# Kernel tuning notes

Hardware: AMD Instinct MI355X
Metric: run time of the kernel (lower is better)

## Reference

```python
import jax, jax.numpy as jnp
import numpy as np

DIM = 512
NUM_HEADS = 8
HEAD_DIM = DIM // NUM_HEADS
EPS = 1e-05
BETA_INIT, TEMP_INIT, SHARP_INIT = 1.0, 0.5, 4.0


def setup_inputs() -> dict:
    key = jax.random.key(0)
    ks = jax.random.split(key, 9)
    b, t = 2, 1024
    s = 1.0 / np.sqrt(DIM)
    inp = {
        "x": jax.random.normal(ks[0], (b, t, DIM), dtype=jnp.float32),
        "wq_k": jax.random.normal(ks[1], (DIM, DIM), dtype=jnp.float32) * s,
        "wq_b": jnp.zeros((DIM,), dtype=jnp.float32),
        "wk_k": jax.random.normal(ks[2], (DIM, DIM), dtype=jnp.float32) * s,
        "wk_b": jnp.zeros((DIM,), dtype=jnp.float32),
        "wv_k": jax.random.normal(ks[3], (DIM, DIM), dtype=jnp.float32) * s,
        "wv_b": jnp.zeros((DIM,), dtype=jnp.float32),
        "wo_k": jax.random.normal(ks[4], (DIM, DIM), dtype=jnp.float32) * s,
        "wo_b": jnp.zeros((DIM,), dtype=jnp.float32),
        "log_beta": jnp.full((NUM_HEADS,), np.log(BETA_INIT), dtype=jnp.float32),
        "log_temp": jnp.full((NUM_HEADS,), np.log(TEMP_INIT), dtype=jnp.float32),
        "log_sharp": jnp.full((NUM_HEADS,), np.log(SHARP_INIT), dtype=jnp.float32),
    }
    return inp


def _softplus(x, beta):
    return (1.0 / beta) * jnp.log(1.0 + jnp.exp(beta * x))


def _combine(a, b):
    # log-domain combine: elements m (b,h,t,n), log_N (b,h,t,p,n), log_D (b,h,t,n)
    m_x, ln_x, ld_x = a
    m_y, ln_y, ld_y = b
    m_new = jnp.maximum(m_x, m_y)
    dx = m_x - m_new
    dy = m_y - m_new
    # note: (..., None) broadcast onto (b,h,t,p,n) works because p == n == HEAD_DIM
    ln_new = jnp.logaddexp(ln_x + dx[..., None], ln_y + dy[..., None])
    ld_new = jnp.logaddexp(ld_x + dx, ld_y + dy)
    return (m_new, ln_new, ld_new)


def reference(x, wq_k, wq_b, wk_k, wk_b, wv_k, wv_b, wo_k, wo_b,
              log_beta, log_temp, log_sharp):
    b, t, _ = x.shape
    q = (x @ wq_k + wq_b).reshape(b, t, NUM_HEADS, HEAD_DIM).transpose(0, 2, 1, 3)
    k = (x @ wk_k + wk_b).reshape(b, t, NUM_HEADS, HEAD_DIM).transpose(0, 2, 1, 3)
    v = (x @ wv_k + wv_b).reshape(b, t, NUM_HEADS, HEAD_DIM).transpose(0, 2, 1, 3)

    beta = jnp.exp(log_beta)[:, None, None]   # (h,1,1)
    temp = jnp.exp(log_temp)[:, None, None]
    sharp = jnp.exp(log_sharp)[:, None, None]

    q = q / temp
    k = k / temp
    Qf = _softplus(q, beta)  # (b,h,t,n)
    Kf = _softplus(k, beta)

    m0 = jnp.log(Kf + EPS)                         # (b,h,t,n)
    N0 = jnp.einsum('bhtp,bhtn->bhtpn', v, Kf)     # (b,h,t,p,n)
    D0 = Kf                                        # (b,h,t,n)

    m_c, N_c, D_c = jax.lax.associative_scan(_combine, (m0, N0, D0), axis=2)

    Y_num = jnp.einsum('bhtp,bhtpq->bhtq', Qf, N_c)
    Y_den = jnp.einsum('bhtp,bhtp->bht', Qf, D_c)
    Y = Y_num / (Y_den[..., None] + EPS)           # (b,h,t,n)
    Y = jnp.sign(Y) * jnp.abs(Y) ** sharp

    pos = (jnp.arange(1, t + 1, dtype=Y.dtype) / t).reshape(1, 1, t, 1)
    Y = Y * pos

    Y = Y.transpose(0, 2, 1, 3).reshape(b, t, DIM)
    return Y @ wo_k + wo_b
```

## Files before the change

### kernel.cpp

```cpp
#include <hip/hip_runtime.h>
#include <hip/hip_bf16.h>
#include <math.h>

#define DIM 512
#define NH 8
#define HD 64
#define TT 1024
#define CH 64
#define CL 16
#define EPSF 1e-5f
#define LN2F 0.69314718056f
#define LOG2EF 1.44269504089f

typedef unsigned short ushort_t;
typedef __attribute__((ext_vector_type(8))) short bf16x8;
typedef __attribute__((ext_vector_type(4))) float f32x4;

__device__ __forceinline__ float fexp2(float x) { return __builtin_amdgcn_exp2f(x); }
__device__ __forceinline__ float flog2(float x) { return __builtin_amdgcn_logf(x); }

__device__ __forceinline__ ushort_t f2bf(float f) {
    union { float f; unsigned u; } v; v.f = f;
    unsigned r = v.u + 0x7FFFu + ((v.u >> 16) & 1u);
    return (ushort_t)(r >> 16);
}
__device__ __forceinline__ float bf2f(ushort_t h) {
    union { unsigned u; float f; } v; v.u = ((unsigned)h) << 16;
    return v.f;
}

#define NXB 1024
__launch_bounds__(256)
__global__ void k_cvt(const float* __restrict__ x, ushort_t* __restrict__ xh,
                      ushort_t* __restrict__ xl,
                      const float* __restrict__ wq, const float* __restrict__ wk,
                      const float* __restrict__ wv, const float* __restrict__ wo,
                      ushort_t* __restrict__ wTh, ushort_t* __restrict__ wTl,
                      ushort_t* __restrict__ wTo)
{
    if (blockIdx.x < NXB) {
        int i = (blockIdx.x * 256 + threadIdx.x) * 4;
        float4 v = *(const float4*)&x[i];
        ushort4 h, l;
        h.x = f2bf(v.x); l.x = f2bf(v.x - bf2f(h.x));
        h.y = f2bf(v.y); l.y = f2bf(v.y - bf2f(h.y));
        h.z = f2bf(v.z); l.z = f2bf(v.z - bf2f(h.z));
        h.w = f2bf(v.w); l.w = f2bf(v.w - bf2f(h.w));
        *(ushort4*)&xh[i] = h;
        *(ushort4*)&xl[i] = l;
        return;
    }
    const int bid = blockIdx.x - NXB;
    const int mat = bid >> 5;
    const int rest = bid & 31;
    const int ky = rest >> 3, nx = rest & 7;
    const float* w = (mat == 0) ? wq : (mat == 1) ? wk : (mat == 2) ? wv : wo;
    const int n  = nx * 64 + (threadIdx.x & 63);
    const int k0 = ky * 128 + (threadIdx.x >> 6) * 32;

    ushort_t hb[32], lb[32];
#pragma unroll
    for (int j = 0; j < 32; j++) {
        float v = w[(size_t)(k0 + j) * DIM + n];
        hb[j] = f2bf(v);
        lb[j] = f2bf(v - bf2f(hb[j]));
    }
    if (mat < 3) {
        ushort_t* dh = wTh + (size_t)mat * DIM * DIM + (size_t)n * DIM + k0;
        ushort_t* dl = wTl + (size_t)mat * DIM * DIM + (size_t)n * DIM + k0;
#pragma unroll
        for (int j = 0; j < 8; j++) {
            ushort4 th = { hb[4*j], hb[4*j+1], hb[4*j+2], hb[4*j+3] };
            ushort4 tl = { lb[4*j], lb[4*j+1], lb[4*j+2], lb[4*j+3] };
            *(ushort4*)&dh[4*j] = th;
            *(ushort4*)&dl[4*j] = tl;
        }
    } else {
        ushort_t* dh = wTo + (size_t)n * DIM + k0;
#pragma unroll
        for (int j = 0; j < 8; j++) {
            ushort4 th = { hb[4*j], hb[4*j+1], hb[4*j+2], hb[4*j+3] };
            *(ushort4*)&dh[4*j] = th;
        }
    }
}

__launch_bounds__(256, 4)
__global__ void k_gemm_qkv(const ushort_t* __restrict__ xh, const ushort_t* __restrict__ xl,
                           const ushort_t* __restrict__ wTh, const ushort_t* __restrict__ wTl,
                           const float* __restrict__ bq, const float* __restrict__ bk,
                           const float* __restrict__ bv,
                           const float* __restrict__ lbeta, const float* __restrict__ ltemp,
                           float* __restrict__ Qf2, float* __restrict__ Kf,
                           float* __restrict__ Vv2)
{
    const int z = blockIdx.z, h = blockIdx.x;
    const int rowBase = blockIdx.y * 64;
    const int colBase = h * 64;
    const float* bias = (z == 0) ? bq : (z == 1) ? bk : bv;

    __shared__ __align__(16) ushort_t lds[2][4][2048];

    const int tid = threadIdx.x;
    const int l = tid & 63, wv = tid >> 6;
    const int m = l & 15, g = l >> 4;
    const int wr = wv & 1, wc = wv >> 1;

    const int rl = tid >> 2, cc = tid & 3;
    const int ci = ((rl >> 4) * 64 + cc * 16 + (rl & 15)) * 8;
    const ushort_t* gAh = xh + (size_t)(rowBase + rl) * DIM + cc * 8;
    const ushort_t* gAl = xl + (size_t)(rowBase + rl) * DIM + cc * 8;
    const ushort_t* gBh = wTh + (size_t)z * DIM * DIM + (size_t)(colBase + rl) * DIM + cc * 8;
    const ushort_t* gBl = wTl + (size_t)z * DIM * DIM + (size_t)(colBase + rl) * DIM + cc * 8;

    f32x4 acc[2][2] = { { {0,0,0,0}, {0,0,0,0} }, { {0,0,0,0}, {0,0,0,0} } };

    {
        bf16x8 a0 = *(const bf16x8*)gAh;
        bf16x8 a1 = *(const bf16x8*)gAl;
        bf16x8 b0 = *(const bf16x8*)gBh;
        bf16x8 b1 = *(const bf16x8*)gBl;
        *(bf16x8*)&lds[0][0][ci] = a0;
        *(bf16x8*)&lds[0][1][ci] = a1;
        *(bf16x8*)&lds[0][2][ci] = b0;
        *(bf16x8*)&lds[0][3][ci] = b1;
    }
    __syncthreads();

    for (int it = 0; it < 16; ++it) {
        const int cur = it & 1;
        bf16x8 nAh, nAl, nBh, nBl;
        if (it < 15) {
            const int K = (it + 1) * 32;
            nAh = *(const bf16x8*)(gAh + K);
            nAl = *(const bf16x8*)(gAl + K);
            nBh = *(const bf16x8*)(gBh + K);
            nBl = *(const bf16x8*)(gBl + K);
        }
        bf16x8 ah[2], al[2], bh[2], bl[2];
#pragma unroll
        for (int rf = 0; rf < 2; rf++) {
            ah[rf] = *(const bf16x8*)&lds[cur][0][((wr * 2 + rf) * 64 + l) * 8];
            al[rf] = *(const bf16x8*)&lds[cur][1][((wr * 2 + rf) * 64 + l) * 8];
        }
#pragma unroll
        for (int cf = 0; cf < 2; cf++) {
            bh[cf] = *(const bf16x8*)&lds[cur][2][((wc * 2 + cf) * 64 + l) * 8];
            bl[cf] = *(const bf16x8*)&lds[cur][3][((wc * 2 + cf) * 64 + l) * 8];
        }
#pragma unroll
        for (int rf = 0; rf < 2; rf++)
#pragma unroll
            for (int cf = 0; cf < 2; cf++) {
                acc[rf][cf] = __builtin_amdgcn_mfma_f32_16x16x32_bf16(ah[rf], bh[cf], acc[rf][cf], 0, 0, 0);
                acc[rf][cf] = __builtin_amdgcn_mfma_f32_16x16x32_bf16(al[rf], bh[cf], acc[rf][cf], 0, 0, 0);
                acc[rf][cf] = __builtin_amdgcn_mfma_f32_16x16x32_bf16(ah[rf], bl[cf], acc[rf][cf], 0, 0, 0);
            }
        if (it < 15) {
            const int nxt = cur ^ 1;
            *(bf16x8*)&lds[nxt][0][ci] = nAh;
            *(bf16x8*)&lds[nxt][1][ci] = nAl;
            *(bf16x8*)&lds[nxt][2][ci] = nBh;
            *(bf16x8*)&lds[nxt][3][ci] = nBl;
            __syncthreads();
        }
    }

    if (z == 2) {
#pragma unroll
        for (int rf = 0; rf < 2; rf++)
#pragma unroll
            for (int cf = 0; cf < 2; cf++) {
                int c = wc * 32 + cf * 16 + m;
                float bval = bias[colBase + c];
#pragma unroll
                for (int r = 0; r < 4; r++) {
                    int rr = rowBase + wr * 32 + rf * 16 + g * 4 + r;
                    int bb = rr >> 10, t = rr & (TT - 1);
                    Vv2[(((size_t)(bb * NH + h)) * TT + t) * HD + c] = (acc[rf][cf][r] + bval) * LOG2EF;
                }
            }
    } else {
        float beta = expf(lbeta[h]);
        float itemp = 1.0f / expf(ltemp[h]);
        float oscale = (z == 0) ? (LN2F / beta) : (1.0f / beta);
        float* __restrict__ dst = (z == 0) ? Qf2 : Kf;
#pragma unroll
        for (int rf = 0; rf < 2; rf++)
#pragma unroll
            for (int cf = 0; cf < 2; cf++) {
                int c = wc * 32 + cf * 16 + m;
                float bval = bias[colBase + c];
#pragma unroll
                for (int r = 0; r < 4; r++) {
                    int rr = rowBase + wr * 32 + rf * 16 + g * 4 + r;
                    int bb = rr >> 10, t = rr & (TT - 1);
                    float val = (acc[rf][cf][r] + bval) * itemp;
                    float zz = beta * val;
                    float sp = (fmaxf(zz, 0.f) + log1pf(expf(-fabsf(zz)))) * oscale;
                    dst[(((size_t)(bb * NH + h)) * TT + t) * HD + c] = sp;
                }
            }
    }
}

__launch_bounds__(256)
__global__ void k_chunk_reduce(const float* __restrict__ Kf, const float* __restrict__ Vv2,
                               float* __restrict__ aA, float* __restrict__ aD,
                               float* __restrict__ aCM)
{
    const int c = blockIdx.x >> 1, qh = blockIdx.x & 1;
    const int bh = blockIdx.z * NH + blockIdx.y;
    const int tid = threadIdx.x;

    __shared__ __align__(16) float sK[CL * HD];
    __shared__ __align__(16) float sV2[CL * HD];
    __shared__ __align__(16) float sM02[CL * HD];

    size_t base = ((size_t)bh * TT + (size_t)c * CL) * HD;
    const float4* K4 = (const float4*)(Kf + base);
    const float4* V4 = (const float4*)(Vv2 + base);
    {
        int f = tid;
        float4 kv = K4[f];
        ((float4*)sK)[f] = kv;
        float4 mm;
        mm.x = flog2(kv.x + EPSF); mm.y = flog2(kv.y + EPSF);
        mm.z = flog2(kv.z + EPSF); mm.w = flog2(kv.w + EPSF);
        ((float4*)sM02)[f] = mm;
        ((float4*)sV2)[f] = V4[f];
    }
    __syncthreads();

    const int p = tid & 63, qo = tid >> 6;
    const int q0 = qh * 32 + qo * 8;
    float A[8] = {};
    float AD = 0.f, cmx = 0.f;
    const bool doD = (qh == 0) && (tid < 64);

#pragma unroll
    for (int s = 0; s < CL; s++) {
        float vp = sV2[s * HD + p];
        float mp = sM02[s * HD + p];
        float4 ka = *(const float4*)&sK[s * HD + q0];
        float4 kb = *(const float4*)&sK[s * HD + q0 + 4];
        A[0] += fexp2(fmaf(vp, ka.x, mp));
        A[1] += fexp2(fmaf(vp, ka.y, mp));
        A[2] += fexp2(fmaf(vp, ka.z, mp));
        A[3] += fexp2(fmaf(vp, ka.w, mp));
        A[4] += fexp2(fmaf(vp, kb.x, mp));
        A[5] += fexp2(fmaf(vp, kb.y, mp));
        A[6] += fexp2(fmaf(vp, kb.z, mp));
        A[7] += fexp2(fmaf(vp, kb.w, mp));
        if (doD) {
            float kn = sK[s * HD + tid];
            float ke = kn + EPSF;
            AD += fexp2(kn * LOG2EF) * ke;
            cmx = fmaxf(cmx, ke);
        }
    }

    size_t abase = ((size_t)bh * CH + c) * 4096 + (size_t)p * HD + q0;
    float4 o0 = { A[0], A[1], A[2], A[3] };
    float4 o1 = { A[4], A[5], A[6], A[7] };
    *(float4*)&aA[abase] = o0;
    *(float4*)&aA[abase + 4] = o1;
    if (doD) {
        size_t dbase = ((size_t)bh * CH + c) * HD + tid;
        aD[dbase] = AD; aCM[dbase] = cmx;
    }
}

__global__ void k_scan_agg(float* __restrict__ aA, float* __restrict__ aD,
                           float* __restrict__ aCM, int BH)
{
    int idx = blockIdx.x * 256 + threadIdx.x;
    int nA4 = BH * 1024;
    int nD4 = BH * 16;
    if (idx < nA4) {
        int bh = idx >> 10, pn4 = (idx & 1023) * 4;
        float4 Sr = {0.f, 0.f, 0.f, 0.f};
        for (int c = 0; c < CH; c++) {
            float* p = &aA[((size_t)bh * CH + c) * 4096 + pn4];
            float4 t = *(float4*)p;
            *(float4*)p = Sr;
            Sr.x += t.x; Sr.y += t.y; Sr.z += t.z; Sr.w += t.w;
        }
    } else if (idx < nA4 + nD4) {
        int i = idx - nA4; int bh = i >> 4, n4 = (i & 15) * 4;
        float4 Sr = {0.f, 0.f, 0.f, 0.f};
        for (int c = 0; c < CH; c++) {
            float* p = &aD[((size_t)bh * CH + c) * HD + n4];
            float4 t = *(float4*)p;
            *(float4*)p = Sr;
            Sr.x += t.x; Sr.y += t.y; Sr.z += t.z; Sr.w += t.w;
        }
    } else if (idx < nA4 + 2 * nD4) {
        int i = idx - nA4 - nD4; int bh = i >> 4, n4 = (i & 15) * 4;
        float4 r = {0.f, 0.f, 0.f, 0.f};
        for (int c = 0; c < CH; c++) {
            float* p = &aCM[((size_t)bh * CH + c) * HD + n4];
            float4 t = *(float4*)p;
            *(float4*)p = r;
            r.x = fmaxf(r.x, t.x); r.y = fmaxf(r.y, t.y);
            r.z = fmaxf(r.z, t.z); r.w = fmaxf(r.w, t.w);
        }
    }
}

__launch_bounds__(256)
__global__ void k_chunk_out(const float* __restrict__ Kf, const float* __restrict__ Vv2,
                            const float* __restrict__ Qf2, const float* __restrict__ aA,
                            const float* __restrict__ aD, const float* __restrict__ aCM,
                            const float* __restrict__ lsharp, ushort_t* __restrict__ Ymb)
{
    const int c = blockIdx.x, hh = blockIdx.y, bb = blockIdx.z;
    const int bh = bb * NH + hh;
    const int tid = threadIdx.x;

    __shared__ __align__(16) float sK[CL * HD];
    __shared__ __align__(16) float sV2[CL * HD];
    __shared__ __align__(16) float sM02[CL * HD];
    __shared__ __align__(16) float sQ2[CL * HD];
    __shared__ float sC1[CL], sIV[CL];

    size_t base = ((size_t)bh * TT + (size_t)c * CL) * HD;
    const float4* K4 = (const float4*)(Kf + base);
    const float4* V4 = (const float4*)(Vv2 + base);
    const float4* Q4 = (const float4*)(Qf2 + base);
    {
        int f = tid;
        float4 kv = K4[f];
        ((float4*)sK)[f] = kv;
        float4 mm;
        mm.x = flog2(kv.x + EPSF); mm.y = flog2(kv.y + EPSF);
        mm.z = flog2(kv.z + EPSF); mm.w = flog2(kv.w + EPSF);
        ((float4*)sM02)[f] = mm;
        ((float4*)sV2)[f] = V4[f];
        ((float4*)sQ2)[f] = Q4[f];
    }
    __syncthreads();

    const int lane = tid & 63, w = tid >> 6;
    const int g = lane >> 3, qil = lane & 7;
    const int qA = w * 8 + qil, qB = qA + 32;
    const int p0 = g * 8;

    float A[8], Bq[8];
    size_t abase = ((size_t)bh * CH + c) * 4096;
#pragma unroll
    for (int j = 0; j < 8; j++) {
        A[j]  = aA[abase + (size_t)(p0 + j) * HD + qA];
        Bq[j] = aA[abase + (size_t)(p0 + j) * HD + qB];
    }

    {
        size_t dofs = ((size_t)bh * CH + c) * HD + lane;
        float AD = aD[dofs], cmx = aCM[dofs];
#pragma unroll
        for (int s = 0; s < CL; s++) {
            float kn = sK[s * HD + lane];
            float ke = kn + EPSF;
            AD += fexp2(kn * LOG2EF) * ke;
            cmx = fmaxf(cmx, ke);
            if ((s & 3) == w) {
                float qn = sQ2[s * HD + lane];
                float t1 = qn * flog2(cmx);
                float t2 = qn * flog2(AD);
#pragma unroll
                for (int off = 1; off <= 32; off <<= 1) {
                    t1 += __shfl_xor(t1, off);
                    t2 += __shfl_xor(t2, off);
                }
                if (lane == 0) {
                    sC1[s] = t1;
                    sIV[s] = 1.0f / (t2 - t1 + EPSF);
                }
            }
        }
    }
    __syncthreads();

    const float sharp = expf(lsharp[hh]);
    const float invT = 1.0f / (float)TT;

#pragma unroll 4
    for (int s = 0; s < CL; s++) {
        float kqA = sK[s * HD + qA];
        float kqB = sK[s * HD + qB];
        float pA0 = 0.f, pA1 = 0.f, pB0 = 0.f, pB1 = 0.f;
#pragma unroll
        for (int j4 = 0; j4 < 2; j4++) {
            float4 vv = *(const float4*)&sV2[s * HD + p0 + j4 * 4];
            float4 mm = *(const float4*)&sM02[s * HD + p0 + j4 * 4];
            float4 qv = *(const float4*)&sQ2[s * HD + p0 + j4 * 4];
#define STEP(comp, jj, PA, PB) { \
            A[jj]  += fexp2(fmaf(vv.comp, kqA, mm.comp)); \
            PA = fmaf(qv.comp, flog2(A[jj]), PA); \
            Bq[jj] += fexp2(fmaf(vv.comp, kqB, mm.comp)); \
            PB = fmaf(qv.comp, flog2(Bq[jj]), PB); }
            STEP(x, j4 * 4 + 0, pA0, pB0)
            STEP(y, j4 * 4 + 1, pA1, pB1)
            STEP(z, j4 * 4 + 2, pA0, pB0)
            STEP(w, j4 * 4 + 3, pA1, pB1)
#undef STEP
        }
        float partA = pA0 + pA1;
        float partB = pB0 + pB1;
        partA += __shfl_xor(partA, 8);
        partA += __shfl_xor(partA, 16);
        partA += __shfl_xor(partA, 32);
        partB += __shfl_xor(partB, 8);
        partB += __shfl_xor(partB, 16);
        partB += __shfl_xor(partB, 32);

        float c1v = sC1[s], iv = sIV[s];
        int tg = c * CL + s;
        float scale = (float)(tg + 1) * invT;
        float yA = (partA - c1v) * iv;
        float yB = (partB - c1v) * iv;
        float oA = copysignf(fexp2(sharp * flog2(fabsf(yA))), yA) * scale;
        float oB = copysignf(fexp2(sharp * flog2(fabsf(yB))), yB) * scale;
        if (g == 0) {
            ushort_t* yrow = Ymb + ((size_t)(bb * TT + tg)) * DIM + hh * HD;
            yrow[qA] = f2bf(oA);
            yrow[qB] = f2bf(oB);
        }
    }
}

__launch_bounds__(256, 4)
__global__ void k_gemm_out(const ushort_t* __restrict__ Ymb, const ushort_t* __restrict__ wTo,
                           const float* __restrict__ bias, float* __restrict__ out)
{
    const int colBase = blockIdx.x * 64;
    const int rowBase = blockIdx.y * 32;

    __shared__ __align__(16) ushort_t sA[2][1024];
    __shared__ __align__(16) ushort_t sB[2][2048];

    const int tid = threadIdx.x;
    const int l = tid & 63, wv = tid >> 6;
    const int m = l & 15, g = l >> 4;
    const int wr = wv & 1, wc = wv >> 1;

    const int rlB = tid >> 2, ccB = tid & 3;
    const int ciB = ((rlB >> 4) * 64 + ccB * 16 + (rlB & 15)) * 8;
    const ushort_t* gB = wTo + (size_t)(colBase + rlB) * DIM + ccB * 8;
    const int rlA = (tid & 127) >> 2, ccA = tid & 3;
    const int ciA = ((rlA >> 4) * 64 + ccA * 16 + (rlA & 15)) * 8;
    const ushort_t* gA = Ymb + (size_t)(rowBase + rlA) * DIM + ccA * 8;
    const bool doA = tid < 128;

    f32x4 acc[2] = { {0,0,0,0}, {0,0,0,0} };

    {
        bf16x8 b0 = *(const bf16x8*)gB;
        *(bf16x8*)&sB[0][ciB] = b0;
        if (doA) {
            bf16x8 a0 = *(const bf16x8*)gA;
            *(bf16x8*)&sA[0][ciA] = a0;
        }
    }
    __syncthreads();

    for (int it = 0; it < 16; ++it) {
        const int cur = it & 1;
        bf16x8 nA, nB;
        if (it < 15) {
            const int K = (it + 1) * 32;
            nB = *(const bf16x8*)(gB + K);
            if (doA) nA = *(const bf16x8*)(gA + K);
        }
        bf16x8 a = *(const bf16x8*)&sA[cur][(wr * 64 + l) * 8];
#pragma unroll
        for (int n = 0; n < 2; n++) {
            bf16x8 b = *(const bf16x8*)&sB[cur][((wc * 2 + n) * 64 + l) * 8];
            acc[n] = __builtin_amdgcn_mfma_f32_16x16x32_bf16(a, b, acc[n], 0, 0, 0);
        }
        if (it < 15) {
            const int nxt = cur ^ 1;
            *(bf16x8*)&sB[nxt][ciB] = nB;
            if (doA) *(bf16x8*)&sA[nxt][ciA] = nA;
            __syncthreads();
        }
    }

#pragma unroll
    for (int n = 0; n < 2; n++) {
        int c = colBase + wc * 32 + n * 16 + m;
        float bval = bias[c];
#pragma unroll
        for (int r = 0; r < 4; r++) {
            int rr = rowBase + wr * 16 + g * 4 + r;
            out[(size_t)rr * DIM + c] = acc[n][r] + bval;
        }
    }
}

extern "C" void kernel_launch(void* const* d_in, const int* in_sizes, int n_in,
                              void* d_out, int out_size, void* d_ws, size_t ws_size,
                              hipStream_t stream)
{
    const float* x  = (const float*)d_in[0];
    const float* wq = (const float*)d_in[1];
    const float* bq = (const float*)d_in[2];
    const float* wk = (const float*)d_in[3];
    const float* bk = (const float*)d_in[4];
    const float* wv = (const float*)d_in[5];
    const float* bv = (const float*)d_in[6];
    const float* wo = (const float*)d_in[7];
    const float* bo = (const float*)d_in[8];
    const float* lb = (const float*)d_in[9];
    const float* lt = (const float*)d_in[10];
    const float* ls = (const float*)d_in[11];

    const int B  = in_sizes[0] / (TT * DIM);
    const int BH = B * NH;

    float* ws = (float*)d_ws;
    const size_t nQ = (size_t)BH * TT * HD;
    float* Qf2 = ws;
    float* Kf  = Qf2 + nQ;
    float* Vv2 = Kf + nQ;
    float* region = Vv2 + nQ;

    ushort_t* xh  = (ushort_t*)region;
    ushort_t* xl  = xh + (size_t)B * TT * DIM;
    ushort_t* wTh = (ushort_t*)(region + (size_t)B * TT * DIM);
    ushort_t* wTl = wTh + (size_t)3 * DIM * DIM;
    ushort_t* Ymb = (ushort_t*)region;
    float* aA  = region + (size_t)B * TT * DIM;
    float* aD  = aA  + (size_t)BH * CH * 4096;
    float* aCM = aD  + (size_t)BH * CH * HD;
    ushort_t* wTo = (ushort_t*)(aCM + (size_t)BH * CH * HD);

    k_cvt<<<NXB + 128, 256, 0, stream>>>(x, xh, xl, wq, wk, wv, wo, wTh, wTl, wTo);

    dim3 g1(NH, (B * TT) / 64, 3);
    k_gemm_qkv<<<g1, 256, 0, stream>>>(xh, xl, wTh, wTl, bq, bk, bv, lb, lt, Qf2, Kf, Vv2);

    dim3 g2(CH * 2, NH, B);
    k_chunk_reduce<<<g2, 256, 0, stream>>>(Kf, Vv2, aA, aD, aCM);

    int ntot = BH * 1024 + 2 * BH * 16;
    k_scan_agg<<<(ntot + 255) / 256, 256, 0, stream>>>(aA, aD, aCM, BH);

    dim3 g4(CH, NH, B);
    k_chunk_out<<<g4, 256, 0, stream>>>(Kf, Vv2, Qf2, aA, aD, aCM, ls, Ymb);

    dim3 g6(DIM / 64, (B * TT) / 32);
    k_gemm_out<<<g6, 256, 0, stream>>>(Ymb, wTo, bo, (float*)d_out);
}
```

Before: 89.05 us.

## Store chunk state in bf16 and process two chunks per chunk_out block

Chunk-level aggregates aA are now stored as bf16 in chunk_reduce, scan_agg and chunk_out, halving traffic on the largest intermediate buffer. chunk_out now handles two chunks per block, with two waves per chunk and each lane computing four q columns, writing ushort4 outputs. This cuts memory bandwidth and improves per-thread ILP, at the cost of bf16 rounding in the running prefix sums, which could hurt accuracy, and fewer blocks in flight.

```diff
diff --git a/kernel.cpp b/kernel.cpp
--- a/kernel.cpp
+++ b/kernel.cpp
@@ -206,7 +206,7 @@
 
 __launch_bounds__(256)
 __global__ void k_chunk_reduce(const float* __restrict__ Kf, const float* __restrict__ Vv2,
-                               float* __restrict__ aA, float* __restrict__ aD,
+                               ushort_t* __restrict__ aAb, float* __restrict__ aD,
                                float* __restrict__ aCM)
 {
     const int c = blockIdx.x >> 1, qh = blockIdx.x & 1;
@@ -261,33 +261,38 @@
     }
 
     size_t abase = ((size_t)bh * CH + c) * 4096 + (size_t)p * HD + q0;
-    float4 o0 = { A[0], A[1], A[2], A[3] };
-    float4 o1 = { A[4], A[5], A[6], A[7] };
-    *(float4*)&aA[abase] = o0;
-    *(float4*)&aA[abase + 4] = o1;
+    bf16x8 o;
+#pragma unroll
+    for (int j = 0; j < 8; j++) o[j] = (short)f2bf(A[j]);
+    *(bf16x8*)&aAb[abase] = o;
     if (doD) {
         size_t dbase = ((size_t)bh * CH + c) * HD + tid;
         aD[dbase] = AD; aCM[dbase] = cmx;
     }
 }
 
-__global__ void k_scan_agg(float* __restrict__ aA, float* __restrict__ aD,
+__global__ void k_scan_agg(ushort_t* __restrict__ aAb, float* __restrict__ aD,
                            float* __restrict__ aCM, int BH)
 {
     int idx = blockIdx.x * 256 + threadIdx.x;
-    int nA4 = BH * 1024;
+    int nA8 = BH * 512;
     int nD4 = BH * 16;
-    if (idx < nA4) {
-        int bh = idx >> 10, pn4 = (idx & 1023) * 4;
-        float4 Sr = {0.f, 0.f, 0.f, 0.f};
+    if (idx < nA8) {
+        int bh = idx >> 9, pn8 = (idx & 511) * 8;
+        float Sr[8] = {};
         for (int c = 0; c < CH; c++) {
-            float* p = &aA[((size_t)bh * CH + c) * 4096 + pn4];
-            float4 t = *(float4*)p;
-            *(float4*)p = Sr;
-            Sr.x += t.x; Sr.y += t.y; Sr.z += t.z; Sr.w += t.w;
-        }
-    } else if (idx < nA4 + nD4) {
-        int i = idx - nA4; int bh = i >> 4, n4 = (i & 15) * 4;
+            ushort_t* p = &aAb[((size_t)bh * CH + c) * 4096 + pn8];
+            bf16x8 t = *(bf16x8*)p;
+            bf16x8 o;
+#pragma unroll
+            for (int i = 0; i < 8; i++) {
+                o[i] = (short)f2bf(Sr[i]);
+                Sr[i] += bf2f((ushort_t)t[i]);
+            }
+            *(bf16x8*)p = o;
+        }
+    } else if (idx < nA8 + nD4) {
+        int i = idx - nA8; int bh = i >> 4, n4 = (i & 15) * 4;
         float4 Sr = {0.f, 0.f, 0.f, 0.f};
         for (int c = 0; c < CH; c++) {
             float* p = &aD[((size_t)bh * CH + c) * HD + n4];
@@ -295,8 +300,8 @@
             *(float4*)p = Sr;
             Sr.x += t.x; Sr.y += t.y; Sr.z += t.z; Sr.w += t.w;
         }
-    } else if (idx < nA4 + 2 * nD4) {
-        int i = idx - nA4 - nD4; int bh = i >> 4, n4 = (i & 15) * 4;
+    } else if (idx < nA8 + 2 * nD4) {
+        int i = idx - nA8 - nD4; int bh = i >> 4, n4 = (i & 15) * 4;
         float4 r = {0.f, 0.f, 0.f, 0.f};
         for (int c = 0; c < CH; c++) {
             float* p = &aCM[((size_t)bh * CH + c) * HD + n4];
@@ -310,26 +315,27 @@
 
 __launch_bounds__(256)
 __global__ void k_chunk_out(const float* __restrict__ Kf, const float* __restrict__ Vv2,
-                            const float* __restrict__ Qf2, const float* __restrict__ aA,
+                            const float* __restrict__ Qf2, const ushort_t* __restrict__ aAb,
                             const float* __restrict__ aD, const float* __restrict__ aCM,
                             const float* __restrict__ lsharp, ushort_t* __restrict__ Ymb)
 {
-    const int c = blockIdx.x, hh = blockIdx.y, bb = blockIdx.z;
+    const int c0 = blockIdx.x * 2, hh = blockIdx.y, bb = blockIdx.z;
     const int bh = bb * NH + hh;
     const int tid = threadIdx.x;
 
-    __shared__ __align__(16) float sK[CL * HD];
-    __shared__ __align__(16) float sV2[CL * HD];
-    __shared__ __align__(16) float sM02[CL * HD];
-    __shared__ __align__(16) float sQ2[CL * HD];
-    __shared__ float sC1[CL], sIV[CL];
-
-    size_t base = ((size_t)bh * TT + (size_t)c * CL) * HD;
+    __shared__ __align__(16) float sK[2 * CL * HD];
+    __shared__ __align__(16) float sV2[2 * CL * HD];
+    __shared__ __align__(16) float sM02[2 * CL * HD];
+    __shared__ __align__(16) float sQ2[2 * CL * HD];
+    __shared__ float sC1[2][CL], sIV[2][CL];
+
+    size_t base = ((size_t)bh * TT + (size_t)c0 * CL) * HD;
     const float4* K4 = (const float4*)(Kf + base);
     const float4* V4 = (const float4*)(Vv2 + base);
     const float4* Q4 = (const float4*)(Qf2 + base);
-    {
-        int f = tid;
+#pragma unroll
+    for (int r = 0; r < 2; r++) {
+        int f = tid + 256 * r;
         float4 kv = K4[f];
         ((float4*)sK)[f] = kv;
         float4 mm;
@@ -342,29 +348,33 @@
     __syncthreads();
 
     const int lane = tid & 63, w = tid >> 6;
+    const int cl = w >> 1, wsub = w & 1;
+    const int cc = c0 + cl;
     const int g = lane >> 3, qil = lane & 7;
-    const int qA = w * 8 + qil, qB = qA + 32;
+    const int qBase = wsub * 32 + qil * 4;
     const int p0 = g * 8;
-
-    float A[8], Bq[8];
-    size_t abase = ((size_t)bh * CH + c) * 4096;
+    const int lbase = cl * CL * HD;
+
+    float A[8][4];
+    size_t abase = ((size_t)bh * CH + cc) * 4096;
 #pragma unroll
     for (int j = 0; j < 8; j++) {
-        A[j]  = aA[abase + (size_t)(p0 + j) * HD + qA];
-        Bq[j] = aA[abase + (size_t)(p0 + j) * HD + qB];
+        ushort4 av = *(const ushort4*)&aAb[abase + (size_t)(p0 + j) * HD + qBase];
+        A[j][0] = bf2f(av.x); A[j][1] = bf2f(av.y);
+        A[j][2] = bf2f(av.z); A[j][3] = bf2f(av.w);
     }
 
     {
-        size_t dofs = ((size_t)bh * CH + c) * HD + lane;
+        size_t dofs = ((size_t)bh * CH + cc) * HD + lane;
         float AD = aD[dofs], cmx = aCM[dofs];
 #pragma unroll
         for (int s = 0; s < CL; s++) {
-            float kn = sK[s * HD + lane];
+            float kn = sK[lbase + s * HD + lane];
             float ke = kn + EPSF;
             AD += fexp2(kn * LOG2EF) * ke;
             cmx = fmaxf(cmx, ke);
-            if ((s & 3) == w) {
-                float qn = sQ2[s * HD + lane];
+            if ((s & 1) == wsub) {
+                float qn = sQ2[lbase + s * HD + lane];
                 float t1 = qn * flog2(cmx);
                 float t2 = qn * flog2(AD);
 #pragma unroll
@@ -373,8 +383,8 @@
                     t2 += __shfl_xor(t2, off);
                 }
                 if (lane == 0) {
-                    sC1[s] = t1;
-                    sIV[s] = 1.0f / (t2 - t1 + EPSF);
+                    sC1[cl][s] = t1;
+                    sIV[cl][s] = 1.0f / (t2 - t1 + EPSF);
                 }
             }
         }
@@ -386,45 +396,48 @@
 
 #pragma unroll 4
     for (int s = 0; s < CL; s++) {
-        float kqA = sK[s * HD + qA];
-        float kqB = sK[s * HD + qB];
-        float pA0 = 0.f, pA1 = 0.f, pB0 = 0.f, pB1 = 0.f;
+        float4 kq = *(const float4*)&sK[lbase + s * HD + qBase];
+        float part[4] = {0.f, 0.f, 0.f, 0.f};
 #pragma unroll
         for (int j4 = 0; j4 < 2; j4++) {
-            float4 vv = *(const float4*)&sV2[s * HD + p0 + j4 * 4];
-            float4 mm = *(const float4*)&sM02[s * HD + p0 + j4 * 4];
-            float4 qv = *(const float4*)&sQ2[s * HD + p0 + j4 * 4];
-#define STEP(comp, jj, PA, PB) { \
-            A[jj]  += fexp2(fmaf(vv.comp, kqA, mm.comp)); \
-            PA = fmaf(qv.comp, flog2(A[jj]), PA); \
-            Bq[jj] += fexp2(fmaf(vv.comp, kqB, mm.comp)); \
-            PB = fmaf(qv.comp, flog2(Bq[jj]), PB); }
-            STEP(x, j4 * 4 + 0, pA0, pB0)
-            STEP(y, j4 * 4 + 1, pA1, pB1)
-            STEP(z, j4 * 4 + 2, pA0, pB0)
-            STEP(w, j4 * 4 + 3, pA1, pB1)
-#undef STEP
-        }
-        float partA = pA0 + pA1;
-        float partB = pB0 + pB1;
-        partA += __shfl_xor(partA, 8);
-        partA += __shfl_xor(partA, 16);
-        partA += __shfl_xor(partA, 32);
-        partB += __shfl_xor(partB, 8);
-        partB += __shfl_xor(partB, 16);
-        partB += __shfl_xor(partB, 32);
-
-        float c1v = sC1[s], iv = sIV[s];
-        int tg = c * CL + s;
-        float scale = (float)(tg + 1) * invT;
-        float yA = (partA - c1v) * iv;
-        float yB = (partB - c1v) * iv;
-        float oA = copysignf(fexp2(sharp * flog2(fabsf(yA))), yA) * scale;
-        float oB = copysignf(fexp2(sharp * flog2(fabsf(yB))), yB) * scale;
+            float4 vv = *(const float4*)&sV2[lbase + s * HD + p0 + j4 * 4];
+            float4 mm = *(const float4*)&sM02[lbase + s * HD + p0 + j4 * 4];
+            float4 qv = *(const float4*)&sQ2[lbase + s * HD + p0 + j4 * 4];
+#define STEPC(comp, jj) { \
+            A[jj][0] += fexp2(fmaf(vv.comp, kq.x, mm.comp)); \
+            A[jj][1] += fexp2(fmaf(vv.comp, kq.y, mm.comp)); \
+            A[jj][2] += fexp2(fmaf(vv.comp, kq.z, mm.comp)); \
+            A[jj][3] += fexp2(fmaf(vv.comp, kq.w, mm.comp)); \
+            part[0] = fmaf(qv.comp, flog2(A[jj][0]), part[0]); \
+            part[1] = fmaf(qv.comp, flog2(A[jj][1]), part[1]); \
+            part[2] = fmaf(qv.comp, flog2(A[jj][2]), part[2]); \
+            part[3] = fmaf(qv.comp, flog2(A[jj][3]), part[3]); }
+            STEPC(x, j4 * 4 + 0)
+            STEPC(y, j4 * 4 + 1)
+            STEPC(z, j4 * 4 + 2)
+            STEPC(w, j4 * 4 + 3)
+#undef STEPC
+        }
+#pragma unroll
+        for (int qi = 0; qi < 4; qi++) {
+            part[qi] += __shfl_xor(part[qi], 8);
+            part[qi] += __shfl_xor(part[qi], 16);
+            part[qi] += __shfl_xor(part[qi], 32);
+        }
         if (g == 0) {
-            ushort_t* yrow = Ymb + ((size_t)(bb * TT + tg)) * DIM + hh * HD;
-            yrow[qA] = f2bf(oA);
-            yrow[qB] = f2bf(oB);
+            float c1v = sC1[cl][s], iv = sIV[cl][s];
+            int tg = cc * CL + s;
+            float scale = (float)(tg + 1) * invT;
+            ushort4 o;
+            float y0 = (part[0] - c1v) * iv;
+            float y1 = (part[1] - c1v) * iv;
+            float y2 = (part[2] - c1v) * iv;
+            float y3 = (part[3] - c1v) * iv;
+            o.x = f2bf(copysignf(fexp2(sharp * flog2(fabsf(y0))), y0) * scale);
+            o.y = f2bf(copysignf(fexp2(sharp * flog2(fabsf(y1))), y1) * scale);
+            o.z = f2bf(copysignf(fexp2(sharp * flog2(fabsf(y2))), y2) * scale);
+            o.w = f2bf(copysignf(fexp2(sharp * flog2(fabsf(y3))), y3) * scale);
+            *(ushort4*)&Ymb[((size_t)(bb * TT + tg)) * DIM + hh * HD + qBase] = o;
         }
     }
 }
@@ -530,8 +543,8 @@
     ushort_t* wTh = (ushort_t*)(region + (size_t)B * TT * DIM);
     ushort_t* wTl = wTh + (size_t)3 * DIM * DIM;
     ushort_t* Ymb = (ushort_t*)region;
-    float* aA  = region + (size_t)B * TT * DIM;
-    float* aD  = aA  + (size_t)BH * CH * 4096;
+    ushort_t* aAb = (ushort_t*)(region + (size_t)B * TT * DIM);
+    float* aD  = region + (size_t)B * TT * DIM + (size_t)BH * CH * 2048;
     float* aCM = aD  + (size_t)BH * CH * HD;
     ushort_t* wTo = (ushort_t*)(aCM + (size_t)BH * CH * HD);
 
@@ -541,13 +554,13 @@
     k_gemm_qkv<<<g1, 256, 0, stream>>>(xh, xl, wTh, wTl, bq, bk, bv, lb, lt, Qf2, Kf, Vv2);
 
     dim3 g2(CH * 2, NH, B);
-    k_chunk_reduce<<<g2, 256, 0, stream>>>(Kf, Vv2, aA, aD, aCM);
-
-    int ntot = BH * 1024 + 2 * BH * 16;
-    k_scan_agg<<<(ntot + 255) / 256, 256, 0, stream>>>(aA, aD, aCM, BH);
-
-    dim3 g4(CH, NH, B);
-    k_chunk_out<<<g4, 256, 0, stream>>>(Kf, Vv2, Qf2, aA, aD, aCM, ls, Ymb);
+    k_chunk_reduce<<<g2, 256, 0, stream>>>(Kf, Vv2, aAb, aD, aCM);
+
+    int ntot = BH * 512 + 2 * BH * 16;
+    k_scan_agg<<<(ntot + 255) / 256, 256, 0, stream>>>(aAb, aD, aCM, BH);
+
+    dim3 g4(CH / 2, NH, B);
+    k_chunk_out<<<g4, 256, 0, stream>>>(Kf, Vv2, Qf2, aAb, aD, aCM, ls, Ymb);
 
     dim3 g6(DIM / 64, (B * TT) / 32);
     k_gemm_out<<<g6, 256, 0, stream>>>(Ymb, wTo, bo, (float*)d_out);
```

Measured after the change: 96.15 us. +8.0%, slower.

## Split chunk-output kernel across two blocks per chunk by output column half

Applied to the files above, without the earlier changes.

The chunk-output kernel now launches twice as many blocks, each handling 32 of the 64 output columns instead of every thread computing two columns. This halves per-thread transcendental work and register use and adds parallelism (1024 to 2048 blocks). The tail computation is also moved under the g==0 branch. The cost is that each block redundantly reloads the K/V/Q tiles and recomputes the per-step prefix statistics.

```diff
diff --git a/kernel.cpp b/kernel.cpp
--- a/kernel.cpp
+++ b/kernel.cpp
@@ -314,7 +314,8 @@
                             const float* __restrict__ aD, const float* __restrict__ aCM,
                             const float* __restrict__ lsharp, ushort_t* __restrict__ Ymb)
 {
-    const int c = blockIdx.x, hh = blockIdx.y, bb = blockIdx.z;
+    const int c = blockIdx.x >> 1, qh = blockIdx.x & 1;
+    const int hh = blockIdx.y, bb = blockIdx.z;
     const int bh = bb * NH + hh;
     const int tid = threadIdx.x;
 
@@ -343,16 +344,14 @@
 
     const int lane = tid & 63, w = tid >> 6;
     const int g = lane >> 3, qil = lane & 7;
-    const int qA = w * 8 + qil, qB = qA + 32;
+    const int qA = qh * 32 + w * 8 + qil;
     const int p0 = g * 8;
 
-    float A[8], Bq[8];
+    float A[8];
     size_t abase = ((size_t)bh * CH + c) * 4096;
 #pragma unroll
-    for (int j = 0; j < 8; j++) {
-        A[j]  = aA[abase + (size_t)(p0 + j) * HD + qA];
-        Bq[j] = aA[abase + (size_t)(p0 + j) * HD + qB];
-    }
+    for (int j = 0; j < 8; j++)
+        A[j] = aA[abase + (size_t)(p0 + j) * HD + qA];
 
     {
         size_t dofs = ((size_t)bh * CH + c) * HD + lane;
@@ -387,44 +386,33 @@
 #pragma unroll 4
     for (int s = 0; s < CL; s++) {
         float kqA = sK[s * HD + qA];
-        float kqB = sK[s * HD + qB];
-        float pA0 = 0.f, pA1 = 0.f, pB0 = 0.f, pB1 = 0.f;
+        float pA0 = 0.f, pA1 = 0.f;
 #pragma unroll
         for (int j4 = 0; j4 < 2; j4++) {
             float4 vv = *(const float4*)&sV2[s * HD + p0 + j4 * 4];
             float4 mm = *(const float4*)&sM02[s * HD + p0 + j4 * 4];
             float4 qv = *(const float4*)&sQ2[s * HD + p0 + j4 * 4];
-#define STEP(comp, jj, PA, PB) { \
-            A[jj]  += fexp2(fmaf(vv.comp, kqA, mm.comp)); \
-            PA = fmaf(qv.comp, flog2(A[jj]), PA); \
-            Bq[jj] += fexp2(fmaf(vv.comp, kqB, mm.comp)); \
-            PB = fmaf(qv.comp, flog2(Bq[jj]), PB); }
-            STEP(x, j4 * 4 + 0, pA0, pB0)
-            STEP(y, j4 * 4 + 1, pA1, pB1)
-            STEP(z, j4 * 4 + 2, pA0, pB0)
-            STEP(w, j4 * 4 + 3, pA1, pB1)
+#define STEP(comp, jj, PA) { \
+            A[jj] += fexp2(fmaf(vv.comp, kqA, mm.comp)); \
+            PA = fmaf(qv.comp, flog2(A[jj]), PA); }
+            STEP(x, j4 * 4 + 0, pA0)
+            STEP(y, j4 * 4 + 1, pA1)
+            STEP(z, j4 * 4 + 2, pA0)
+            STEP(w, j4 * 4 + 3, pA1)
 #undef STEP
         }
         float partA = pA0 + pA1;
-        float partB = pB0 + pB1;
         partA += __shfl_xor(partA, 8);
         partA += __shfl_xor(partA, 16);
         partA += __shfl_xor(partA, 32);
-        partB += __shfl_xor(partB, 8);
-        partB += __shfl_xor(partB, 16);
-        partB += __shfl_xor(partB, 32);
-
-        float c1v = sC1[s], iv = sIV[s];
-        int tg = c * CL + s;
-        float scale = (float)(tg + 1) * invT;
-        float yA = (partA - c1v) * iv;
-        float yB = (partB - c1v) * iv;
-        float oA = copysignf(fexp2(sharp * flog2(fabsf(yA))), yA) * scale;
-        float oB = copysignf(fexp2(sharp * flog2(fabsf(yB))), yB) * scale;
+
         if (g == 0) {
-            ushort_t* yrow = Ymb + ((size_t)(bb * TT + tg)) * DIM + hh * HD;
-            yrow[qA] = f2bf(oA);
-            yrow[qB] = f2bf(oB);
+            float c1v = sC1[s], iv = sIV[s];
+            int tg = c * CL + s;
+            float scale = (float)(tg + 1) * invT;
+            float yA = (partA - c1v) * iv;
+            float oA = copysignf(fexp2(sharp * flog2(fabsf(yA))), yA) * scale;
+            Ymb[((size_t)(bb * TT + tg)) * DIM + hh * HD + qA] = f2bf(oA);
         }
     }
 }
@@ -546,7 +534,7 @@
     int ntot = BH * 1024 + 2 * BH * 16;
     k_scan_agg<<<(ntot + 255) / 256, 256, 0, stream>>>(aA, aD, aCM, BH);
 
-    dim3 g4(CH, NH, B);
+    dim3 g4(CH * 2, NH, B);
     k_chunk_out<<<g4, 256, 0, stream>>>(Kf, Vv2, Qf2, aA, aD, aCM, ls, Ymb);
 
     dim3 g6(DIM / 64, (B * TT) / 32);
```

Result: slower. 91.18 us (+2.4%).
